# Performance work log

Measured on AMD Instinct MI355X. Metric: run time of the kernel, lower is better.

The kernel has to match this reference:

```python
import jax, jax.numpy as jnp
import numpy as np

B, L, D = 32, 1024, 256
G = 3 * D


def _gelu(x):
    return jax.nn.gelu(x, approximate=False)


def _start_embed(x, w0, b0, w1, b1, w2, b2):
    out = x @ w0.T + b0
    res = out
    out = _gelu(out)
    out = _gelu(out @ w1.T + b1)
    out = out @ w2.T + b2
    return out + res


def _gru_layer(x_seq, h0, w_ih, w_hh, b_ih, b_hh):
    # x_seq: [L, B, in]; torch GRU gate order: r, z, n
    xp = jnp.einsum('lbi,gi->lbg', x_seq, w_ih) + b_ih  # [L, B, 3D]
    def step(h, xpt):
        hp = h @ w_hh.T + b_hh
        xr, xz, xn = jnp.split(xpt, 3, axis=-1)
        hr, hz, hn = jnp.split(hp, 3, axis=-1)
        r = jax.nn.sigmoid(xr + hr)
        z = jax.nn.sigmoid(xz + hz)
        n = jnp.tanh(xn + r * hn)
        h_new = (1.0 - z) * n + z * h
        return h_new, h_new
    _, outs = jax.lax.scan(step, h0, xp)
    return outs  # [L, B, D]


def _p(k, shape):
    return jax.random.normal(k, shape, jnp.float32) * 0.05


def setup_inputs():
    key = jax.random.key(0)
    ks = iter(jax.random.split(key, 32))
    inp = {}
    inp['noisy_enc'] = jax.random.normal(next(ks), (B, L), jnp.float32)
    inp['mask'] = jnp.ones((B, L), jnp.float32)
    inp['trg_seq'] = jax.random.randint(next(ks), (B, L), 0, 2)
    inp['se_w0'] = _p(next(ks), (D, L)); inp['se_b0'] = _p(next(ks), (D,))
    inp['se_w1'] = _p(next(ks), (D, D)); inp['se_b1'] = _p(next(ks), (D,))
    inp['se_w2'] = _p(next(ks), (D, D)); inp['se_b2'] = _p(next(ks), (D,))
    inp['w_ih0'] = _p(next(ks), (G, 1)); inp['w_hh0'] = _p(next(ks), (G, D))
    inp['b_ih0'] = _p(next(ks), (G,));   inp['b_hh0'] = _p(next(ks), (G,))
    inp['w_ih1'] = _p(next(ks), (G, D)); inp['w_hh1'] = _p(next(ks), (G, D))
    inp['b_ih1'] = _p(next(ks), (G,));   inp['b_hh1'] = _p(next(ks), (G,))
    inp['attn_w1'] = _p(next(ks), (D, D)); inp['attn_b1'] = _p(next(ks), (D,))
    inp['comb_w'] = _p(next(ks), (D, 3 * D)); inp['comb_b'] = _p(next(ks), (D,))
    inp['dec_w0'] = _p(next(ks), (D, D)); inp['dec_b0'] = _p(next(ks), (D,))
    inp['dec_w1'] = _p(next(ks), (D, D)); inp['dec_b1'] = _p(next(ks), (D,))
    inp['dec_w2'] = _p(next(ks), (1, D)); inp['dec_b2'] = _p(next(ks), (1,))
    return inp


def reference(noisy_enc, mask, trg_seq,
              se_w0, se_b0, se_w1, se_b1, se_w2, se_b2,
              w_ih0, w_hh0, b_ih0, b_hh0, w_ih1, w_hh1, b_ih1, b_hh1,
              attn_w1, attn_b1, comb_w, comb_b,
              dec_w0, dec_b0, dec_w1, dec_b1, dec_w2, dec_b2):
    # shift target right, prepend start token = 1
    trg = jnp.concatenate(
        [jnp.ones((B, 1), jnp.float32), trg_seq[:, :-1].astype(jnp.float32)], axis=-1)
    x = trg.T[:, :, None]  # [L, B, 1]

    sh = _start_embed(noisy_enc, se_w0, se_b0, se_w1, se_b1, se_w2, se_b2)  # [B, D]
    o0 = _gru_layer(x, sh, w_ih0, w_hh0, b_ih0, b_hh0)
    o1 = _gru_layer(o0, sh, w_ih1, w_hh1, b_ih1, b_hh1)
    outs = jnp.transpose(o1, (1, 0, 2))  # [B, L, D]

    # causal dot-product attention (diagonal masked out, row 0 zeroed)
    modif = outs @ attn_w1.T + attn_b1
    attn_logits = jnp.einsum('bld,bmd->blm', outs, modif)
    causal = jnp.triu(jnp.full((L, L), -1e16, jnp.float32))
    attn = jax.nn.softmax(attn_logits + causal, axis=-1)
    attn = attn * (jnp.arange(L) > 0).astype(attn.dtype)[None, :, None]
    ctx = jnp.einsum('blm,bmd->bld', attn, outs)

    sh_b = jnp.broadcast_to(sh[:, None, :], (B, L, D))
    cat = jnp.concatenate([ctx, outs, sh_b], axis=-1)  # [B, L, 3D]
    dec = jnp.tanh(cat @ comb_w.T + comb_b)
    h = _gelu(dec @ dec_w0.T + dec_b0)
    h = _gelu(h @ dec_w1.T + dec_b1)
    logits = h @ dec_w2.T + dec_b2  # [B, L, 1]

    p = jax.nn.sigmoid(logits)
    output = jnp.concatenate([1.0 - p, p], axis=-1)  # [B, L, 2]
    decoded_msg_bits = jnp.sign(logits)
    return (output, decoded_msg_bits, mask, logits)
```

## Files before the change

### kernel.cpp

```cpp
#include <hip/hip_runtime.h>
#include <math.h>

#define NROWS 32768

typedef float v4 __attribute__((ext_vector_type(4)));
typedef _Float16 h2 __attribute__((ext_vector_type(2)));
typedef _Float16 f16x8 __attribute__((ext_vector_type(8)));
typedef float f32x4 __attribute__((ext_vector_type(4)));

__device__ __forceinline__ float geluf(float x){ return 0.5f*x*(1.0f+erff(x*0.70710678118654752f)); }

__device__ __forceinline__ float fexp2(float x){
#if __has_builtin(__builtin_amdgcn_exp2f)
    return __builtin_amdgcn_exp2f(x);
#else
    return exp2f(x);
#endif
}
__device__ __forceinline__ float frcp(float x){
#if __has_builtin(__builtin_amdgcn_rcpf)
    return __builtin_amdgcn_rcpf(x);
#else
    return 1.0f/x;
#endif
}
#define LOG2E 1.44269504088896f
__device__ __forceinline__ float fexp(float x){ return fexp2(x*LOG2E); }
__device__ __forceinline__ float sigm(float x){ return frcp(1.0f + fexp2(-LOG2E*x)); }
__device__ __forceinline__ float ftanh(float x){ return 1.0f - 2.0f*frcp(fexp2(2.0f*LOG2E*x) + 1.0f); }

__device__ __forceinline__ float dot2(h2 a, h2 b, float c){
#if __has_builtin(__builtin_amdgcn_fdot2)
    return __builtin_amdgcn_fdot2(a, b, c, false);
#else
    return c + (float)a.x*(float)b.x + (float)a.y*(float)b.y;
#endif
}
__device__ __forceinline__ h2 cvt2(float2 a){ return h2{(_Float16)a.x, (_Float16)a.y}; }

__device__ __forceinline__ void wg_barrier(){
    asm volatile("s_waitcnt lgkmcnt(0)" ::: "memory");
    __builtin_amdgcn_s_barrier();
    __builtin_amdgcn_sched_barrier(0);
}

__global__ __launch_bounds__(256) void k_start_embed(
    const float* __restrict__ ne, const float* __restrict__ w0, const float* __restrict__ b0,
    const float* __restrict__ w1, const float* __restrict__ b1,
    const float* __restrict__ w2, const float* __restrict__ b2,
    float* __restrict__ sh)
{
    __shared__ __align__(16) float encL[1024];
    __shared__ __align__(16) float g1[256];
    __shared__ __align__(16) float g2[256];
    int b = blockIdx.x, t = threadIdx.x;
    for (int i = t; i < 1024; i += 256) encL[i] = ne[b*1024 + i];
    __syncthreads();
    const float4* wr = (const float4*)(w0 + (size_t)t*1024);
    const float4* e4 = (const float4*)encL;
    float a0=0,a1=0,a2=0,a3=0;
    #pragma unroll 8
    for (int k = 0; k < 256; ++k){ float4 w = wr[k], e = e4[k];
        a0 += w.x*e.x; a1 += w.y*e.y; a2 += w.z*e.z; a3 += w.w*e.w; }
    float t1 = a0+a1+a2+a3 + b0[t];
    float res = t1;
    g1[t] = geluf(t1);
    __syncthreads();
    const float4* w1r = (const float4*)(w1 + (size_t)t*256);
    const float4* g14 = (const float4*)g1;
    a0=a1=a2=a3=0.f;
    #pragma unroll 8
    for (int k = 0; k < 64; ++k){ float4 w = w1r[k], e = g14[k];
        a0 += w.x*e.x; a1 += w.y*e.y; a2 += w.z*e.z; a3 += w.w*e.w; }
    g2[t] = geluf(a0+a1+a2+a3 + b1[t]);
    __syncthreads();
    const float4* w2r = (const float4*)(w2 + (size_t)t*256);
    const float4* g24 = (const float4*)g2;
    a0=a1=a2=a3=0.f;
    #pragma unroll 8
    for (int k = 0; k < 64; ++k){ float4 w = w2r[k], e = g24[k];
        a0 += w.x*e.x; a1 += w.y*e.y; a2 += w.z*e.z; a3 += w.w*e.w; }
    sh[b*256 + t] = a0+a1+a2+a3 + b2[t] + res;
}

__device__ __forceinline__ int hperm(int dim){
    return ((dim >> 3) & 7)*32 + ((dim >> 6) << 3) + (dim & 7);
}

template<int LAYER>
__global__ __launch_bounds__(512) void k_gru3(
    const float* __restrict__ w_hh, const float* __restrict__ b_hh,
    const float* __restrict__ w_ih0, const float* __restrict__ b_ih0,
    const _Float16* __restrict__ xp1,
    const int*   __restrict__ trg,
    const float* __restrict__ sh,
    float* __restrict__ out)
{
    __shared__ __align__(16) float4 wNs[8192];
    __shared__ __align__(16) _Float16 hbuf[2][256];
    __shared__ __align__(16) float bitL[1024];
    int b = blockIdx.x, t = threadIdx.x;
    int d = t >> 1, half = t & 1;

    if (LAYER == 0) {
        #pragma unroll
        for (int i = 0; i < 2; ++i) {
            int idx = t + i*512;
            bitL[idx] = (idx == 0) ? 1.0f : (float)trg[b*1024 + idx - 1];
        }
    }

    {
        const float2* src = (const float2*)(w_hh + (size_t)(512 + d)*256 + half*128);
        #pragma unroll
        for (int kk = 0; kk < 16; ++kk) {
            h2 p0 = cvt2(src[kk*4+0]), p1 = cvt2(src[kk*4+1]);
            h2 p2 = cvt2(src[kk*4+2]), p3 = cvt2(src[kk*4+3]);
            float4 v;
            v.x = __builtin_bit_cast(float, p0); v.y = __builtin_bit_cast(float, p1);
            v.z = __builtin_bit_cast(float, p2); v.w = __builtin_bit_cast(float, p3);
            wNs[kk*512 + t] = v;
        }
    }
    h2 wR[64], wZ[64];
    {
        const float2* wr = (const float2*)(w_hh + (size_t)d*256       + half*128);
        const float2* wz = (const float2*)(w_hh + (size_t)(d+256)*256 + half*128);
        #pragma unroll
        for (int k = 0; k < 64; ++k) { wR[k] = cvt2(wr[k]); wZ[k] = cvt2(wz[k]); }
    }
    float bhr = b_hh[d], bhz = b_hh[256 + d], bhn = b_hh[512 + d];
    float wir=0.f, wiz=0.f, win=0.f, bir=0.f, biz=0.f, bin=0.f;
    if (LAYER == 0) {
        wir = w_ih0[d]; wiz = w_ih0[256 + d]; win = w_ih0[512 + d];
        bir = b_ih0[d]; biz = b_ih0[256 + d]; bin = b_ih0[512 + d];
    }

    float hreg = sh[b*256 + d];
    if (half == 0) hbuf[0][hperm(d)] = (_Float16)hreg;

    float xr = 0.f, xz = 0.f, xn = 0.f;
    if (LAYER == 1) {
        size_t base = (size_t)b*768;
        xr = (float)xp1[base + d]; xz = (float)xp1[base + 256 + d]; xn = (float)xp1[base + 512 + d];
    }
    __syncthreads();

    for (int l = 0; l < 1024; ++l) {
        const float4* hb4 = (const float4*)(&hbuf[l & 1][0]);
        float ar = 0.f, az = 0.f, an = 0.f;
        #pragma unroll
        for (int kk = 0; kk < 16; ++kk) {
            float4 hv = hb4[(kk & 7)*4 + half*2 + (kk >> 3)];
            float4 wv = wNs[kk*512 + t];
            h2 h0 = __builtin_bit_cast(h2, hv.x);
            h2 h1 = __builtin_bit_cast(h2, hv.y);
            h2 hc = __builtin_bit_cast(h2, hv.z);
            h2 h3 = __builtin_bit_cast(h2, hv.w);
            ar = dot2(wR[4*kk+0], h0, ar); ar = dot2(wR[4*kk+1], h1, ar);
            ar = dot2(wR[4*kk+2], hc, ar); ar = dot2(wR[4*kk+3], h3, ar);
            az = dot2(wZ[4*kk+0], h0, az); az = dot2(wZ[4*kk+1], h1, az);
            az = dot2(wZ[4*kk+2], hc, az); az = dot2(wZ[4*kk+3], h3, az);
            an = dot2(__builtin_bit_cast(h2, wv.x), h0, an);
            an = dot2(__builtin_bit_cast(h2, wv.y), h1, an);
            an = dot2(__builtin_bit_cast(h2, wv.z), hc, an);
            an = dot2(__builtin_bit_cast(h2, wv.w), h3, an);
        }
        ar += __shfl_xor(ar, 1);
        az += __shfl_xor(az, 1);
        an += __shfl_xor(an, 1);
        if (LAYER == 0) {
            float bit = bitL[l];
            xr = bir + bit*wir; xz = biz + bit*wiz; xn = bin + bit*win;
        }
        float r = sigm(xr + ar + bhr);
        float z = sigm(xz + az + bhz);
        float n = ftanh(xn + r*(an + bhn));
        hreg = (1.0f - z)*n + z*hreg;
        if (half == 0) {
            hbuf[(l + 1) & 1][hperm(d)] = (_Float16)hreg;
        } else {
            size_t oidx = (LAYER == 0) ? (((size_t)l*32 + b)*256 + d)
                                       : (((size_t)b*1024 + l)*256 + d);
            out[oidx] = hreg;
        }
        if (LAYER == 1) {
            int ln = (l < 1023) ? (l + 1) : 1023;
            size_t base = ((size_t)ln*32 + b)*768;
            xr = (float)xp1[base + d]; xz = (float)xp1[base + 256 + d]; xn = (float)xp1[base + 512 + d];
        }
        wg_barrier();
    }
}

__global__ __launch_bounds__(256, 3) void k_gemm_mfma(
    const float* __restrict__ A, const float* __restrict__ B,
    const float* __restrict__ bias, float* __restrict__ C,
    int M, int N, int K, int act, int aMode, int outHalf,
    const float* __restrict__ A1, const float* __restrict__ A2)
{
    __shared__ __align__(16) _Float16 As[128][40];
    __shared__ __align__(16) _Float16 Bs[128][40];
    int nbn = N >> 7;
    int bx = blockIdx.x % nbn, by = blockIdx.x / nbn;
    int m0 = by << 7, n0 = bx << 7;
    int t = threadIdx.x;
    int w = t >> 6, l = t & 63;
    int wm = w >> 1, wn = w & 1;
    int lc = l & 15, lg = l >> 4;
    f32x4 acc[4][4] = {};
    for (int kt = 0; kt < K; kt += 32) {
        __syncthreads();
        #pragma unroll
        for (int p = 0; p < 4; ++p) {
            int slot = t + p*256;
            int m = slot >> 3, kc = slot & 7;
            int gk = kt + kc*4;
            float4 va;
            if (aMode == 0) {
                va = *(const float4*)(A + (size_t)(m0+m)*K + gk);
            } else {
                int part = gk >> 8, kk = gk & 255;
                const float* P = (part == 0) ? A : ((part == 1) ? A1 : A2);
                int row = (part == 2) ? ((m0+m) >> 10) : (m0+m);
                va = *(const float4*)(P + (size_t)row*256 + kk);
            }
            h2 pa; pa[0] = (_Float16)va.x; pa[1] = (_Float16)va.y;
            h2 pb; pb[0] = (_Float16)va.z; pb[1] = (_Float16)va.w;
            *(float2*)(&As[m][kc*4]) = make_float2(__builtin_bit_cast(float, pa),
                                                   __builtin_bit_cast(float, pb));
            float4 vb = *(const float4*)(B + (size_t)(n0+m)*K + gk);
            h2 qa; qa[0] = (_Float16)vb.x; qa[1] = (_Float16)vb.y;
            h2 qb; qb[0] = (_Float16)vb.z; qb[1] = (_Float16)vb.w;
            *(float2*)(&Bs[m][kc*4]) = make_float2(__builtin_bit_cast(float, qa),
                                                   __builtin_bit_cast(float, qb));
        }
        __syncthreads();
        f16x8 af[4], bf[4];
        #pragma unroll
        for (int mt = 0; mt < 4; ++mt)
            af[mt] = *(const f16x8*)(&As[wm*64 + mt*16 + lc][lg*8]);
        #pragma unroll
        for (int nt = 0; nt < 4; ++nt)
            bf[nt] = *(const f16x8*)(&Bs[wn*64 + nt*16 + lc][lg*8]);
        #pragma unroll
        for (int mt = 0; mt < 4; ++mt)
            #pragma unroll
            for (int nt = 0; nt < 4; ++nt)
                acc[mt][nt] = __builtin_amdgcn_mfma_f32_16x16x32_f16(af[mt], bf[nt], acc[mt][nt], 0, 0, 0);
    }
    #pragma unroll
    for (int nt = 0; nt < 4; ++nt) {
        int col = n0 + wn*64 + nt*16 + lc;
        float bv = bias[col];
        #pragma unroll
        for (int mt = 0; mt < 4; ++mt) {
            int rbase = m0 + wm*64 + mt*16 + lg*4;
            #pragma unroll
            for (int r = 0; r < 4; ++r) {
                float v = acc[mt][nt][r] + bv;
                if (act == 1) v = geluf(v);
                else if (act == 2) v = ftanh(v);
                if (outHalf) ((_Float16*)C)[(size_t)(rbase + r)*N + col] = (_Float16)v;
                else         C[(size_t)(rbase + r)*N + col] = v;
            }
        }
    }
}

__global__ __launch_bounds__(256) void k_attn_mfma(
    const float* __restrict__ outs, const float* __restrict__ modif, float* __restrict__ ctx)
{
    __shared__ __align__(16) _Float16 Qsh[64][264];
    __shared__ __align__(16) _Float16 Qsl[64][264];
    __shared__ __align__(16) _Float16 Ksh[32][264];
    __shared__ __align__(16) _Float16 Ksl[32][264];
    __shared__ __align__(16) _Float16 Vt[256][40];
    __shared__ __align__(16) _Float16 sP[4][16][40];
    int b = blockIdx.y, bx = blockIdx.x, l0 = bx << 6, t = threadIdx.x;
    int w = t >> 6, l = t & 63;
    int lc = l & 15, lg = l >> 4;

    #pragma unroll
    for (int p = 0; p < 16; ++p) {
        int i = p*256 + t;
        int row = i >> 6, c4 = i & 63;
        float4 v = *(const float4*)(outs + ((size_t)b*1024 + l0 + row)*256 + c4*4);
        _Float16 hx = (_Float16)v.x, hy = (_Float16)v.y, hz = (_Float16)v.z, hw = (_Float16)v.w;
        h2 pa; pa[0] = hx; pa[1] = hy;
        h2 pb; pb[0] = hz; pb[1] = hw;
        *(float2*)(&Qsh[row][c4*4]) = make_float2(__builtin_bit_cast(float, pa),
                                                  __builtin_bit_cast(float, pb));
        h2 la; la[0] = (_Float16)(v.x - (float)hx); la[1] = (_Float16)(v.y - (float)hy);
        h2 lb; lb[0] = (_Float16)(v.z - (float)hz); lb[1] = (_Float16)(v.w - (float)hw);
        *(float2*)(&Qsl[row][c4*4]) = make_float2(__builtin_bit_cast(float, la),
                                                  __builtin_bit_cast(float, lb));
    }
    __syncthreads();
    f16x8 aqh[8], aql[8];
    #pragma unroll
    for (int kf = 0; kf < 8; ++kf) {
        aqh[kf] = *(const f16x8*)(&Qsh[w + 4*lc][kf*32 + lg*8]);
        aql[kf] = *(const f16x8*)(&Qsl[w + 4*lc][kf*32 + lg*8]);
    }

    f32x4 cacc[16] = {};
    float rowM[4] = {-1e30f, -1e30f, -1e30f, -1e30f};
    float rowL[4] = {0.f, 0.f, 0.f, 0.f};

    int T = 2*bx + 2;
    for (int tt = 0; tt < T; ++tt) {
        int m0 = tt << 5;
        __syncthreads();
        #pragma unroll
        for (int p = 0; p < 8; ++p) {
            int i = p*256 + t;
            int row = i >> 6, c4 = i & 63;
            float4 kv = *(const float4*)(modif + ((size_t)b*1024 + m0 + row)*256 + c4*4);
            _Float16 hx = (_Float16)kv.x, hy = (_Float16)kv.y, hz = (_Float16)kv.z, hw = (_Float16)kv.w;
            h2 pa; pa[0] = hx; pa[1] = hy;
            h2 pb; pb[0] = hz; pb[1] = hw;
            *(float2*)(&Ksh[row][c4*4]) = make_float2(__builtin_bit_cast(float, pa),
                                                      __builtin_bit_cast(float, pb));
            h2 la; la[0] = (_Float16)(kv.x - (float)hx); la[1] = (_Float16)(kv.y - (float)hy);
            h2 lb; lb[0] = (_Float16)(kv.z - (float)hz); lb[1] = (_Float16)(kv.w - (float)hw);
            *(float2*)(&Ksl[row][c4*4]) = make_float2(__builtin_bit_cast(float, la),
                                                      __builtin_bit_cast(float, lb));
            float4 vv = *(const float4*)(outs + ((size_t)b*1024 + m0 + row)*256 + c4*4);
            Vt[c4*4+0][row] = (_Float16)vv.x;
            Vt[c4*4+1][row] = (_Float16)vv.y;
            Vt[c4*4+2][row] = (_Float16)vv.z;
            Vt[c4*4+3][row] = (_Float16)vv.w;
        }
        __syncthreads();
        f32x4 s0 = {0.f,0.f,0.f,0.f}, s1 = {0.f,0.f,0.f,0.f};
        #pragma unroll
        for (int kf = 0; kf < 8; ++kf) {
            f16x8 b0h = *(const f16x8*)(&Ksh[lc][kf*32 + lg*8]);
            f16x8 b0l = *(const f16x8*)(&Ksl[lc][kf*32 + lg*8]);
            f16x8 b1h = *(const f16x8*)(&Ksh[16 + lc][kf*32 + lg*8]);
            f16x8 b1l = *(const f16x8*)(&Ksl[16 + lc][kf*32 + lg*8]);
            s0 = __builtin_amdgcn_mfma_f32_16x16x32_f16(aqh[kf], b0h, s0, 0, 0, 0);
            s0 = __builtin_amdgcn_mfma_f32_16x16x32_f16(aqh[kf], b0l, s0, 0, 0, 0);
            s0 = __builtin_amdgcn_mfma_f32_16x16x32_f16(aql[kf], b0h, s0, 0, 0, 0);
            s1 = __builtin_amdgcn_mfma_f32_16x16x32_f16(aqh[kf], b1h, s1, 0, 0, 0);
            s1 = __builtin_amdgcn_mfma_f32_16x16x32_f16(aqh[kf], b1l, s1, 0, 0, 0);
            s1 = __builtin_amdgcn_mfma_f32_16x16x32_f16(aql[kf], b1h, s1, 0, 0, 0);
        }
        #pragma unroll
        for (int r = 0; r < 4; ++r) {
            int m = lg*4 + r;
            int grow = l0 + w + 4*m;
            float v0 = s0[r], v1 = s1[r];
            if (m0 + lc      >= grow) v0 = -1e30f;
            if (m0 + 16 + lc >= grow) v1 = -1e30f;
            float mx = fmaxf(v0, v1);
            mx = fmaxf(mx, __shfl_xor(mx, 1));
            mx = fmaxf(mx, __shfl_xor(mx, 2));
            mx = fmaxf(mx, __shfl_xor(mx, 4));
            mx = fmaxf(mx, __shfl_xor(mx, 8));
            float nm = fmaxf(rowM[r], mx);
            float sc, p0, p1;
            if (nm < -1e29f) { sc = 1.f; p0 = 0.f; p1 = 0.f; }
            else { sc = fexp(rowM[r] - nm); p0 = fexp(v0 - nm); p1 = fexp(v1 - nm); }
            rowM[r] = nm;
            float ts = p0 + p1;
            ts += __shfl_xor(ts, 1);
            ts += __shfl_xor(ts, 2);
            ts += __shfl_xor(ts, 4);
            ts += __shfl_xor(ts, 8);
            rowL[r] = rowL[r]*sc + ts;
            sP[w][m][lc]      = (_Float16)p0;
            sP[w][m][16 + lc] = (_Float16)p1;
            #pragma unroll
            for (int nt = 0; nt < 16; ++nt) cacc[nt][r] *= sc;
        }
        asm volatile("s_waitcnt lgkmcnt(0)" ::: "memory");
        __builtin_amdgcn_sched_barrier(0);
        f16x8 pa = *(const f16x8*)(&sP[w][lc][lg*8]);
        #pragma unroll
        for (int nt = 0; nt < 16; ++nt) {
            f16x8 bv = *(const f16x8*)(&Vt[nt*16 + lc][lg*8]);
            cacc[nt] = __builtin_amdgcn_mfma_f32_16x16x32_f16(pa, bv, cacc[nt], 0, 0, 0);
        }
    }
    #pragma unroll
    for (int r = 0; r < 4; ++r) {
        int grow = l0 + w + 4*(lg*4 + r);
        float inv = (grow == 0) ? 0.f : 1.f/rowL[r];
        #pragma unroll
        for (int nt = 0; nt < 16; ++nt)
            ctx[((size_t)b*1024 + grow)*256 + nt*16 + lc] = cacc[nt][r]*inv;
    }
}

__global__ __launch_bounds__(256) void k_final(
    const float* __restrict__ h2v, const float* __restrict__ w2, const float* __restrict__ b2,
    const float* __restrict__ mask, float* __restrict__ out)
{
    int i = blockIdx.x*256 + threadIdx.x;
    const float4* h4 = (const float4*)(h2v + (size_t)i*256);
    const float4* w4 = (const float4*)w2;
    float a0=0,a1=0,a2=0,a3=0;
    #pragma unroll 8
    for (int k = 0; k < 64; ++k) {
        float4 h = h4[k], w = w4[k];
        a0 += h.x*w.x; a1 += h.y*w.y; a2 += h.z*w.z; a3 += h.w*w.w;
    }
    float lg = a0+a1+a2+a3 + b2[0];
    float p = sigm(lg);
    out[2*i]     = 1.0f - p;
    out[2*i + 1] = p;
    out[65536  + i] = (lg > 0.f) ? 1.0f : ((lg < 0.f) ? -1.0f : 0.0f);
    out[98304  + i] = mask[i];
    out[131072 + i] = lg;
}

extern "C" void kernel_launch(void* const* d_in, const int* in_sizes, int n_in,
                              void* d_out, int out_size, void* d_ws, size_t ws_size,
                              hipStream_t stream)
{
    const float* ne      = (const float*)d_in[0];
    const float* mask    = (const float*)d_in[1];
    const int*   trg     = (const int*)  d_in[2];
    const float* se_w0   = (const float*)d_in[3];
    const float* se_b0   = (const float*)d_in[4];
    const float* se_w1   = (const float*)d_in[5];
    const float* se_b1   = (const float*)d_in[6];
    const float* se_w2   = (const float*)d_in[7];
    const float* se_b2   = (const float*)d_in[8];
    const float* w_ih0   = (const float*)d_in[9];
    const float* w_hh0   = (const float*)d_in[10];
    const float* b_ih0   = (const float*)d_in[11];
    const float* b_hh0   = (const float*)d_in[12];
    const float* w_ih1   = (const float*)d_in[13];
    const float* w_hh1   = (const float*)d_in[14];
    const float* b_ih1   = (const float*)d_in[15];
    const float* b_hh1   = (const float*)d_in[16];
    const float* attn_w1 = (const float*)d_in[17];
    const float* attn_b1 = (const float*)d_in[18];
    const float* comb_w  = (const float*)d_in[19];
    const float* comb_b  = (const float*)d_in[20];
    const float* dec_w0  = (const float*)d_in[21];
    const float* dec_b0  = (const float*)d_in[22];
    const float* dec_w1  = (const float*)d_in[23];
    const float* dec_b1  = (const float*)d_in[24];
    const float* dec_w2  = (const float*)d_in[25];
    const float* dec_b2  = (const float*)d_in[26];

    float* W    = (float*)d_ws;
    float* sh   = W;
    float* o0   = W + 8192;
    float* xp1f = W + 8396800;
    float* outs = W + 33562624;
    float* modif = o0;
    float* ctx  = xp1f + 8388608;
    float* dec  = xp1f + 16777216;
    float* h1   = outs;
    float* out  = (float*)d_out;

    h1 = o0;
    float* h2b  = xp1f;

    k_start_embed<<<32, 256, 0, stream>>>(ne, se_w0, se_b0, se_w1, se_b1, se_w2, se_b2, sh);
    k_gru3<0><<<32, 512, 0, stream>>>(w_hh0, b_hh0, w_ih0, b_ih0, nullptr, trg, sh, o0);
    k_gemm_mfma<<<1536, 256, 0, stream>>>(o0, w_ih1, b_ih1, xp1f, NROWS, 768, 256, 0, 0, 1, nullptr, nullptr);
    k_gru3<1><<<32, 512, 0, stream>>>(w_hh1, b_hh1, nullptr, nullptr, (const _Float16*)xp1f, trg, sh, outs);
    k_gemm_mfma<<<512, 256, 0, stream>>>(outs, attn_w1, attn_b1, modif, NROWS, 256, 256, 0, 0, 0, nullptr, nullptr);
    { dim3 ag(16, 32); k_attn_mfma<<<ag, 256, 0, stream>>>(outs, modif, ctx); }
    k_gemm_mfma<<<512, 256, 0, stream>>>(ctx, comb_w, comb_b, dec, NROWS, 256, 768, 2, 3, 0, outs, sh);
    k_gemm_mfma<<<512, 256, 0, stream>>>(dec, dec_w0, dec_b0, h1, NROWS, 256, 256, 1, 0, 0, nullptr, nullptr);
    k_gemm_mfma<<<512, 256, 0, stream>>>(h1, dec_w1, dec_b1, h2b, NROWS, 256, 256, 1, 0, 0, nullptr, nullptr);
    k_final<<<128, 256, 0, stream>>>(h2b, dec_w2, dec_b2, mask, out);
}
```

Measured before the change: 2.830 ms.

## Pipeline both GRU layers and input projection in one persistent kernel with flags

```diff
diff --git a/kernel.cpp b/kernel.cpp
--- a/kernel.cpp
+++ b/kernel.cpp
@@ -87,29 +87,113 @@
     return ((dim >> 3) & 7)*32 + ((dim >> 6) << 3) + (dim & 7);
 }
 
-template<int LAYER>
-__global__ __launch_bounds__(512) void k_gru3(
-    const float* __restrict__ w_hh, const float* __restrict__ b_hh,
+__global__ __launch_bounds__(64) void k_zero(unsigned* flags){
+    flags[threadIdx.x] = 0u;
+}
+
+__global__ __launch_bounds__(512) void k_pipe(
+    const float* __restrict__ w_hh0, const float* __restrict__ b_hh0,
     const float* __restrict__ w_ih0, const float* __restrict__ b_ih0,
-    const _Float16* __restrict__ xp1,
-    const int*   __restrict__ trg,
-    const float* __restrict__ sh,
-    float* __restrict__ out)
+    const float* __restrict__ w_hh1, const float* __restrict__ b_hh1,
+    const float* __restrict__ w_ih1v, const float* __restrict__ b_ih1,
+    const int*   __restrict__ trg, const float* __restrict__ sh,
+    float* __restrict__ o0, _Float16* __restrict__ xpf,
+    float* __restrict__ outs, unsigned* __restrict__ flags)
 {
     __shared__ __align__(16) float4 wNs[8192];
     __shared__ __align__(16) _Float16 hbuf[2][256];
     __shared__ __align__(16) float bitL[1024];
-    int b = blockIdx.x, t = threadIdx.x;
+    int role = blockIdx.x >> 5, b = blockIdx.x & 31, t = threadIdx.x;
     int d = t >> 1, half = t & 1;
 
-    if (LAYER == 0) {
+    if (role == 1) {
+        {
+            const float2* src = (const float2*)(w_ih1v + (size_t)(512 + d)*256 + half*128);
+            #pragma unroll
+            for (int kk = 0; kk < 16; ++kk) {
+                h2 p0 = cvt2(src[kk*4+0]), p1 = cvt2(src[kk*4+1]);
+                h2 p2 = cvt2(src[kk*4+2]), p3 = cvt2(src[kk*4+3]);
+                float4 v;
+                v.x = __builtin_bit_cast(float, p0); v.y = __builtin_bit_cast(float, p1);
+                v.z = __builtin_bit_cast(float, p2); v.w = __builtin_bit_cast(float, p3);
+                wNs[kk*512 + t] = v;
+            }
+        }
+        h2 wR[64], wZ[64];
+        {
+            const float2* wr = (const float2*)(w_ih1v + (size_t)d*256       + half*128);
+            const float2* wz = (const float2*)(w_ih1v + (size_t)(d+256)*256 + half*128);
+            #pragma unroll
+            for (int k = 0; k < 64; ++k) { wR[k] = cvt2(wr[k]); wZ[k] = cvt2(wz[k]); }
+        }
+        float bir = b_ih1[d], biz = b_ih1[256 + d], bin = b_ih1[512 + d];
+        _Float16* obuf = (_Float16*)bitL;
+        __syncthreads();
+
+        for (int lc0 = 0; lc0 < 1024; lc0 += 8) {
+            if (t == 0) {
+                unsigned tgt = (unsigned)(lc0 + 8);
+                for (long it = 0; it < 10000000L; ++it) {
+                    if (atomicAdd(&flags[b], 0u) >= tgt) break;
+                    __builtin_amdgcn_s_sleep(2);
+                }
+            }
+            __syncthreads(); __threadfence(); __syncthreads();
+            {
+                int r = t >> 6, c4 = t & 63;
+                float4 v = *(const float4*)(o0 + ((size_t)(lc0 + r)*32 + b)*256 + c4*4);
+                h2 pa; pa[0] = (_Float16)v.x; pa[1] = (_Float16)v.y;
+                h2 pb; pb[0] = (_Float16)v.z; pb[1] = (_Float16)v.w;
+                *(float2*)(&obuf[r*256 + hperm(c4*4)]) = make_float2(
+                    __builtin_bit_cast(float, pa), __builtin_bit_cast(float, pb));
+            }
+            wg_barrier();
+            #pragma unroll 2
+            for (int r = 0; r < 8; ++r) {
+                int ls = lc0 + r;
+                const float4* hb4 = (const float4*)(&obuf[r*256]);
+                float ar = 0.f, az = 0.f, an = 0.f;
+                #pragma unroll
+                for (int kk = 0; kk < 16; ++kk) {
+                    float4 hv = hb4[(kk & 7)*4 + half*2 + (kk >> 3)];
+                    float4 wv = wNs[kk*512 + t];
+                    h2 h0 = __builtin_bit_cast(h2, hv.x);
+                    h2 h1 = __builtin_bit_cast(h2, hv.y);
+                    h2 hc = __builtin_bit_cast(h2, hv.z);
+                    h2 h3 = __builtin_bit_cast(h2, hv.w);
+                    ar = dot2(wR[4*kk+0], h0, ar); ar = dot2(wR[4*kk+1], h1, ar);
+                    ar = dot2(wR[4*kk+2], hc, ar); ar = dot2(wR[4*kk+3], h3, ar);
+                    az = dot2(wZ[4*kk+0], h0, az); az = dot2(wZ[4*kk+1], h1, az);
+                    az = dot2(wZ[4*kk+2], hc, az); az = dot2(wZ[4*kk+3], h3, az);
+                    an = dot2(__builtin_bit_cast(h2, wv.x), h0, an);
+                    an = dot2(__builtin_bit_cast(h2, wv.y), h1, an);
+                    an = dot2(__builtin_bit_cast(h2, wv.z), hc, an);
+                    an = dot2(__builtin_bit_cast(h2, wv.w), h3, an);
+                }
+                ar += __shfl_xor(ar, 1);
+                az += __shfl_xor(az, 1);
+                an += __shfl_xor(an, 1);
+                if (half) {
+                    size_t base = ((size_t)ls*32 + b)*768;
+                    xpf[base + d]       = (_Float16)(ar + bir);
+                    xpf[base + 256 + d] = (_Float16)(az + biz);
+                    xpf[base + 512 + d] = (_Float16)(an + bin);
+                }
+            }
+            __syncthreads(); __threadfence(); __syncthreads();
+            if (t == 0) atomicExch(&flags[32 + b], (unsigned)(lc0 + 8));
+        }
+        return;
+    }
+
+    const float* w_hh = (role == 0) ? w_hh0 : w_hh1;
+    const float* b_hh = (role == 0) ? b_hh0 : b_hh1;
+    if (role == 0)
         #pragma unroll
         for (int i = 0; i < 2; ++i) {
             int idx = t + i*512;
             bitL[idx] = (idx == 0) ? 1.0f : (float)trg[b*1024 + idx - 1];
         }
-    }
-
     {
         const float2* src = (const float2*)(w_hh + (size_t)(512 + d)*256 + half*128);
         #pragma unroll
@@ -131,22 +215,30 @@
     }
     float bhr = b_hh[d], bhz = b_hh[256 + d], bhn = b_hh[512 + d];
     float wir=0.f, wiz=0.f, win=0.f, bir=0.f, biz=0.f, bin=0.f;
-    if (LAYER == 0) {
+    if (role == 0) {
         wir = w_ih0[d]; wiz = w_ih0[256 + d]; win = w_ih0[512 + d];
         bir = b_ih0[d]; biz = b_ih0[256 + d]; bin = b_ih0[512 + d];
     }
-
     float hreg = sh[b*256 + d];
     if (half == 0) hbuf[0][hperm(d)] = (_Float16)hreg;
-
-    float xr = 0.f, xz = 0.f, xn = 0.f;
-    if (LAYER == 1) {
-        size_t base = (size_t)b*768;
-        xr = (float)xp1[base + d]; xz = (float)xp1[base + 256 + d]; xn = (float)xp1[base + 512 + d];
-    }
     __syncthreads();
 
     for (int l = 0; l < 1024; ++l) {
+        float xr = 0.f, xz = 0.f, xn = 0.f;
+        if (role == 2) {
+            if ((l & 7) == 0) {
+                if (t == 0) {
+                    unsigned tgt = (unsigned)(l + 8);
+                    for (long it = 0; it < 10000000L; ++it) {
+                        if (atomicAdd(&flags[32 + b], 0u) >= tgt) break;
+                        __builtin_amdgcn_s_sleep(2);
+                    }
+                }
+                __syncthreads(); __threadfence(); __syncthreads();
+            }
+            size_t base = ((size_t)l*32 + b)*768;
+            xr = (float)xpf[base + d]; xz = (float)xpf[base + 256 + d]; xn = (float)xpf[base + 512 + d];
+        }
         const float4* hb4 = (const float4*)(&hbuf[l & 1][0]);
         float ar = 0.f, az = 0.f, an = 0.f;
         #pragma unroll
@@ -169,7 +261,7 @@
         ar += __shfl_xor(ar, 1);
         az += __shfl_xor(az, 1);
         an += __shfl_xor(an, 1);
-        if (LAYER == 0) {
+        if (role == 0) {
             float bit = bitL[l];
             xr = bir + bit*wir; xz = biz + bit*wiz; xn = bin + bit*win;
         }
@@ -180,16 +272,17 @@
         if (half == 0) {
             hbuf[(l + 1) & 1][hperm(d)] = (_Float16)hreg;
         } else {
-            size_t oidx = (LAYER == 0) ? (((size_t)l*32 + b)*256 + d)
-                                       : (((size_t)b*1024 + l)*256 + d);
-            out[oidx] = hreg;
-        }
-        if (LAYER == 1) {
-            int ln = (l < 1023) ? (l + 1) : 1023;
-            size_t base = ((size_t)ln*32 + b)*768;
-            xr = (float)xp1[base + d]; xz = (float)xp1[base + 256 + d]; xn = (float)xp1[base + 512 + d];
-        }
-        wg_barrier();
+            size_t oidx = (role == 0) ? (((size_t)l*32 + b)*256 + d)
+                                      : (((size_t)b*1024 + l)*256 + d);
+            float* dst = (role == 0) ? o0 : outs;
+            dst[oidx] = hreg;
+        }
+        if (role == 0 && (l & 7) == 7) {
+            __syncthreads(); __threadfence(); __syncthreads();
+            if (t == 0) atomicExch(&flags[b], (unsigned)(l + 1));
+        } else {
+            wg_barrier();
+        }
     }
 }
 
@@ -456,16 +549,16 @@
     float* modif = o0;
     float* ctx  = xp1f + 8388608;
     float* dec  = xp1f + 16777216;
-    float* h1   = outs;
+    unsigned* flags = (unsigned*)(xp1f + 16777216);
+    float* h1   = o0;
+    float* h2b  = xp1f;
     float* out  = (float*)d_out;
 
-    h1 = o0;
-    float* h2b  = xp1f;
-
     k_start_embed<<<32, 256, 0, stream>>>(ne, se_w0, se_b0, se_w1, se_b1, se_w2, se_b2, sh);
-    k_gru3<0><<<32, 512, 0, stream>>>(w_hh0, b_hh0, w_ih0, b_ih0, nullptr, trg, sh, o0);
-    k_gemm_mfma<<<1536, 256, 0, stream>>>(o0, w_ih1, b_ih1, xp1f, NROWS, 768, 256, 0, 0, 1, nullptr, nullptr);
-    k_gru3<1><<<32, 512, 0, stream>>>(w_hh1, b_hh1, nullptr, nullptr, (const _Float16*)xp1f, trg, sh, outs);
+    k_zero<<<1, 64, 0, stream>>>(flags);
+    k_pipe<<<96, 512, 0, stream>>>(w_hh0, b_hh0, w_ih0, b_ih0,
+                                   w_hh1, b_hh1, w_ih1, b_ih1,
+                                   trg, sh, o0, (_Float16*)xp1f, outs, flags);
     k_gemm_mfma<<<512, 256, 0, stream>>>(outs, attn_w1, attn_b1, modif, NROWS, 256, 256, 0, 0, 0, nullptr, nullptr);
     { dim3 ag(16, 32); k_attn_mfma<<<ag, 256, 0, stream>>>(outs, modif, ctx); }
     k_gemm_mfma<<<512, 256, 0, stream>>>(ctx, comb_w, comb_b, dec, NROWS, 256, 768, 2, 3, 0, outs, sh);
```

After: 3.462 ms. +22.3%, slower.
